# Optimization experiments

Measured on AMD Instinct MI355X. Metric: run time of the kernel, lower is better.

Reference implementation:

```python
import jax, jax.numpy as jnp
import numpy as np

H = 16  # num_heads

def _toroidal_bias(S, dtype):
    # float mask: +1.0 at (i, (i-1)%S), (i,i), (i, (i+1)%S); PyTorch ADDS float attn_mask to scores
    eye = jnp.eye(S, dtype=dtype)
    return eye + jnp.roll(eye, 1, axis=1) + jnp.roll(eye, -1, axis=1)

def setup_inputs() -> dict:
    key = jax.random.key(0)
    ks = jax.random.split(key, 7)
    E = 1024
    S, B = 2048, 2
    sc = 0.02
    return {
        "x": jax.random.normal(ks[0], (S, B, E), dtype=jnp.float32),
        "w_tor": jax.random.normal(ks[1], (E, E), dtype=jnp.float32) * sc,
        "b_tor": jax.random.normal(ks[2], (E,), dtype=jnp.float32) * sc,
        "in_proj_w": jax.random.normal(ks[3], (3 * E, E), dtype=jnp.float32) * sc,
        "in_proj_b": jax.random.normal(ks[4], (3 * E,), dtype=jnp.float32) * sc,
        "out_w": jax.random.normal(ks[5], (E, E), dtype=jnp.float32) * sc,
        "out_b": jax.random.normal(ks[6], (E,), dtype=jnp.float32) * sc,
    }

def reference(x, w_tor, b_tor, in_proj_w, in_proj_b, out_w, out_b):
    S, B, E = x.shape
    hd = E // H
    scale = 1.0 / jnp.sqrt(jnp.asarray(hd, dtype=x.dtype))
    # toroidal projection, then fused in_proj (self-attention: q=k=v=x_toroidal)
    xt = x @ w_tor.T + b_tor                      # (S,B,E)
    qkv = xt @ in_proj_w.T + in_proj_b            # (S,B,3E)
    q, k, v = jnp.split(qkv, 3, axis=-1)
    def to_heads(t):
        return t.reshape(S, B, H, hd).transpose(1, 2, 0, 3)  # (B,H,S,hd)
    q, k, v = to_heads(q), to_heads(k), to_heads(v)
    bias = _toroidal_bias(S, x.dtype)             # (S,S) additive float mask
    scores = jnp.einsum('bhqd,bhkd->bhqk', q * scale, k) + bias
    attn = jax.nn.softmax(scores, axis=-1)
    o = jnp.einsum('bhqk,bhkd->bhqd', attn, v)    # (B,H,S,hd)
    o = o.transpose(2, 0, 1, 3).reshape(S, B, E)
    return o @ out_w.T + out_b
```

## Files before the change

kernel.cpp:

```cpp
#include <hip/hip_runtime.h>

#define S_LEN 2048
#define NB    2
#define EMB   1024
#define NH    16
#define HD    64

typedef __bf16 bf16_t;
typedef bf16_t bf16x8 __attribute__((ext_vector_type(8)));
typedef bf16_t bf16x4v __attribute__((ext_vector_type(4)));
typedef float  f32x4  __attribute__((ext_vector_type(4)));
typedef float  f32x16 __attribute__((ext_vector_type(16)));

#define L2E 1.44269504f

__device__ __forceinline__ void g2l16(const void* g, void* l) {
    auto gp = reinterpret_cast<const unsigned int __attribute__((address_space(1)))*>(
        reinterpret_cast<uintptr_t>(g));
    auto lp = reinterpret_cast<unsigned int __attribute__((address_space(3)))*>(
        reinterpret_cast<uintptr_t>(l));
    __builtin_amdgcn_global_load_lds(gp, lp, 16, 0, 0);
}

__device__ __forceinline__ unsigned int pk2(float a, float b) {
    union { unsigned int u; bf16_t h[2]; } r;
    r.h[0] = (bf16_t)a; r.h[1] = (bf16_t)b;
    return r.u;
}

__global__ __launch_bounds__(256) void cast4_f32_bf16(
    const float* __restrict__ s0, bf16_t* __restrict__ d0,
    const float* __restrict__ s1, bf16_t* __restrict__ d1,
    const float* __restrict__ s2, bf16_t* __restrict__ d2,
    const float* __restrict__ s3, bf16_t* __restrict__ d3)
{
    long i = (long)blockIdx.x * 256 + threadIdx.x;
    const float* s; bf16_t* d; long off;
    if (i < 1048576)      { s = s0; d = d0; off = i; }
    else if (i < 1310720) { s = s1; d = d1; off = i - 1048576; }
    else if (i < 2097152) { s = s2; d = d2; off = i - 1310720; }
    else                  { s = s3; d = d3; off = i - 2097152; }
    float4 v = ((const float4*)s)[off];
    bf16x4v o;
    o[0] = (bf16_t)v.x; o[1] = (bf16_t)v.y; o[2] = (bf16_t)v.z; o[3] = (bf16_t)v.w;
    *(bf16x4v*)(d + off * 4) = o;
}

template<int TN, int MODE>
__global__ __launch_bounds__(256) void gemm_bt_bf16(
    const bf16_t* __restrict__ A, const bf16_t* __restrict__ W,
    const float* __restrict__ bias, void* __restrict__ Cout,
    bf16_t* __restrict__ Qp, bf16_t* __restrict__ Kp, bf16_t* __restrict__ Vtp,
    int M, int N, int K)
{
    constexpr int MB = (TN == 128) ? 4 : 2;
    __shared__ __align__(16) bf16_t As[2][128 * 32];
    __shared__ __align__(16) bf16_t Bs[2][TN * 32];

    const int tid  = threadIdx.x;
    const int lane = tid & 63;
    const int w    = tid >> 6;
    const int lm   = lane & 15;
    const int lq   = lane >> 4;
    const long m0  = (long)blockIdx.y * 128;
    const long n0  = (long)blockIdx.x * TN;
    const int wm0  = (TN == 128) ? (w >> 1) * 64 : w * 32;
    const int wn0  = (TN == 128) ? (w & 1) * 64 : 0;

    f32x4 acc[MB][4];
#pragma unroll
    for (int i = 0; i < MB; ++i)
#pragma unroll
        for (int j = 0; j < 4; ++j) acc[i][j] = (f32x4){0.f, 0.f, 0.f, 0.f};

    auto stage = [&](int k0, int buf) {
        bf16_t* asb = &As[buf][0];
        bf16_t* bsb = &Bs[buf][0];
#pragma unroll
        for (int j = 0; j < 2; ++j) {
            int a   = (w * 2 + j) * 64 + lane;
            int row = a >> 2;
            int c   = (a & 3) ^ ((row >> 1) & 3);
            g2l16(A + (m0 + row) * K + k0 + c * 8, asb + (w * 2 + j) * 512);
        }
#pragma unroll
        for (int j = 0; j < TN / 64; ++j) {
            int a   = (w * (TN / 64) + j) * 64 + lane;
            int row = a >> 2;
            int c   = (a & 3) ^ ((row >> 1) & 3);
            g2l16(W + (n0 + row) * K + k0 + c * 8, bsb + (w * (TN / 64) + j) * 512);
        }
    };

    stage(0, 0);
    for (int k0 = 0; k0 < K; k0 += 32) {
        const int cur = (k0 >> 5) & 1;
        asm volatile("s_waitcnt vmcnt(0)" ::: "memory");
        __syncthreads();
        if (k0 + 32 < K) stage(k0 + 32, cur ^ 1);

        bf16x8 af[MB], bfr[4];
#pragma unroll
        for (int mb = 0; mb < MB; ++mb) {
            int r = wm0 + mb * 16 + lm;
            af[mb] = *(const bf16x8*)&As[cur][r * 32 + ((lq ^ ((r >> 1) & 3)) << 3)];
        }
#pragma unroll
        for (int nb = 0; nb < 4; ++nb) {
            int r = wn0 + nb * 16 + lm;
            bfr[nb] = *(const bf16x8*)&Bs[cur][r * 32 + ((lq ^ ((r >> 1) & 3)) << 3)];
        }
#pragma unroll
        for (int mb = 0; mb < MB; ++mb)
#pragma unroll
            for (int nb = 0; nb < 4; ++nb)
                acc[mb][nb] = __builtin_amdgcn_mfma_f32_16x16x32_bf16(
                    af[mb], bfr[nb], acc[mb][nb], 0, 0, 0);
    }

    float b4[4];
#pragma unroll
    for (int nb = 0; nb < 4; ++nb) b4[nb] = bias[n0 + wn0 + nb * 16 + lm];

    if (MODE == 2) {
#pragma unroll
        for (int mb = 0; mb < MB; ++mb) {
            const long mbase = m0 + wm0 + mb * 16 + lq * 4;
#pragma unroll
            for (int nb = 0; nb < 4; ++nb) {
                int n    = (int)n0 + wn0 + nb * 16 + lm;
                int sec  = n >> 10;
                int nloc = n & 1023;
                int h    = nloc >> 6;
                int d    = nloc & 63;
                if (sec == 2) {
                    int s0 = (int)(mbase >> 1) + 0;
#pragma unroll
                    for (int rp = 0; rp < 2; ++rp) {
                        int bh = rp * 16 + h;
                        unsigned int pk = pk2(acc[mb][nb][rp] + b4[nb],
                                              acc[mb][nb][rp + 2] + b4[nb]);
                        *(unsigned int*)&Vtp[((size_t)(bh * 64 + d)) * S_LEN + s0] = pk;
                    }
                } else {
#pragma unroll
                    for (int r = 0; r < 4; ++r) {
                        long m  = mbase + r;
                        int  s  = (int)(m >> 1), b = (int)(m & 1);
                        int  bh = b * 16 + h;
                        float v = acc[mb][nb][r] + b4[nb];
                        if (sec == 0) {
                            Qp[((size_t)(bh * S_LEN + s)) * 64 + d] =
                                (bf16_t)(v * (0.125f * L2E));
                        } else {
                            Kp[((size_t)(bh * S_LEN + s)) * 64 + d] = (bf16_t)v;
                        }
                    }
                }
            }
        }
    } else {
#pragma unroll
        for (int mb = 0; mb < MB; ++mb) {
#pragma unroll
            for (int r = 0; r < 4; ++r) {
                long m = m0 + wm0 + mb * 16 + lq * 4 + r;
#pragma unroll
                for (int nb = 0; nb < 4; ++nb) {
                    int n   = (int)n0 + wn0 + nb * 16 + lm;
                    float v = acc[mb][nb][r] + b4[nb];
                    if (MODE == 0) ((float*)Cout)[m * N + n] = v;
                    else           ((bf16_t*)Cout)[m * N + n] = (bf16_t)v;
                }
            }
        }
    }
}

__global__ __launch_bounds__(256, 2) void attn_mfma(
    const bf16_t* __restrict__ Qb, const bf16_t* __restrict__ Kb,
    const bf16_t* __restrict__ Vtb, bf16_t* __restrict__ O)
{
    __shared__ __align__(16) bf16_t Ks[2][8 * 512];
    __shared__ __align__(16) bf16_t Vts[2][8 * 512];
    __shared__ __align__(16) bf16_t Ps[4][8 * 256];

    const int tid  = threadIdx.x;
    const int lane = tid & 63;
    const int w    = tid >> 6;
    const int bid  = blockIdx.x;
    const int bh   = ((bid & 7) << 2) | (bid >> 7);
    const int qt   = (bid >> 3) & 15;
    const int l5   = lane & 31;
    const int hi   = lane >> 5;

    const int rsub = lane >> 3;
    const int csw  = (lane & 7) ^ rsub;
    int cc[4];
#pragma unroll
    for (int i = 0; i < 4; ++i) cc[i] = ((2 * i + hi) ^ (l5 & 7)) * 8;

    const bf16_t* qrow = Qb + ((size_t)bh * S_LEN + qt * 128 + w * 32 + l5) * 64 + hi * 8;
    bf16x8 qf[4];
#pragma unroll
    for (int ds = 0; ds < 4; ++ds) qf[ds] = *(const bf16x8*)(qrow + ds * 16);

    f32x16 oacc[2];
#pragma unroll
    for (int dh = 0; dh < 2; ++dh)
#pragma unroll
        for (int i = 0; i < 16; ++i) oacc[dh][i] = 0.f;
    float plsum = 0.f;

    auto stageKV = [&](int kt, int buf) {
        bf16_t* ksb = &Ks[buf][0];
        bf16_t* vsb = &Vts[buf][0];
        const bf16_t* kg = Kb + ((size_t)bh * S_LEN + kt * 64) * 64;
        const bf16_t* vg = Vtb + (size_t)bh * 64 * S_LEN + kt * 64;
#pragma unroll
        for (int j = 0; j < 2; ++j) {
            int i = w * 2 + j;
            g2l16(kg + (size_t)(i * 8 + rsub) * 64 + csw * 8,    ksb + i * 512);
            g2l16(vg + (size_t)(i * 8 + rsub) * S_LEN + csw * 8, vsb + i * 512);
        }
    };

    stageKV(0, 0);
    for (int kt = 0; kt < 32; ++kt) {
        const int cur = kt & 1;
        asm volatile("s_waitcnt vmcnt(0)" ::: "memory");
        __syncthreads();
        if (kt < 31) stageKV(kt + 1, cur ^ 1);

        f32x16 sacc[2];
        __builtin_amdgcn_s_setprio(1);
#pragma unroll
        for (int kh = 0; kh < 2; ++kh) {
#pragma unroll
            for (int i = 0; i < 16; ++i) sacc[kh][i] = 0.f;
#pragma unroll
            for (int ds = 0; ds < 4; ++ds) {
                bf16x8 kf = *(const bf16x8*)&Ks[cur][(kh * 32 + l5) * 64 + cc[ds]];
                sacc[kh] = __builtin_amdgcn_mfma_f32_32x32x16_bf16(kf, qf[ds], sacc[kh], 0, 0, 0);
            }
        }
        __builtin_amdgcn_s_setprio(0);

        int ktd = (kt - 2 * qt) & 31;
        if (ktd <= 2 || ktd == 31) {
            int q = qt * 128 + w * 32 + l5;
#pragma unroll
            for (int kh = 0; kh < 2; ++kh)
#pragma unroll
                for (int r = 0; r < 16; ++r) {
                    int key  = kt * 64 + kh * 32 + (r & 3) + 8 * (r >> 2) + 4 * hi;
                    int diff = (key - q) & (S_LEN - 1);
                    if (diff <= 1 || diff == S_LEN - 1) sacc[kh][r] += L2E;
                }
        }

#pragma unroll
        for (int kh = 0; kh < 2; ++kh)
#pragma unroll
            for (int g = 0; g < 4; ++g) {
                bf16x4v pk;
#pragma unroll
                for (int e = 0; e < 4; ++e) {
                    float p = __builtin_amdgcn_exp2f(sacc[kh][g * 4 + e]);
                    plsum += p;
                    pk[e] = (bf16_t)p;
                }
                *(bf16x4v*)&Ps[w][(kh * 4 + g) * 256 + hi * 128 + l5 * 4] = pk;
            }

        bf16x8 pf[4];
#pragma unroll
        for (int ks = 0; ks < 4; ++ks) {
            bf16x4v lo = *(const bf16x4v*)&Ps[w][(2 * ks + hi) * 256 + l5 * 4];
            bf16x4v hb = *(const bf16x4v*)&Ps[w][(2 * ks + hi) * 256 + 128 + l5 * 4];
#pragma unroll
            for (int e = 0; e < 4; ++e) { pf[ks][e] = lo[e]; pf[ks][4 + e] = hb[e]; }
        }
        __builtin_amdgcn_s_setprio(1);
#pragma unroll
        for (int dh = 0; dh < 2; ++dh) {
#pragma unroll
            for (int ks = 0; ks < 4; ++ks) {
                bf16x8 vf = *(const bf16x8*)&Vts[cur][(dh * 32 + l5) * 64 + cc[ks]];
                oacc[dh] = __builtin_amdgcn_mfma_f32_32x32x16_bf16(pf[ks], vf, oacc[dh], 0, 0, 0);
            }
        }
        __builtin_amdgcn_s_setprio(0);
    }

    plsum += __shfl_xor(plsum, 32, 64);
    float* Lw = (float*)&Ps[w][0];
    if (hi == 0) Lw[l5] = plsum;

    float inv16[16];
#pragma unroll
    for (int g = 0; g < 4; ++g) {
        f32x4 lv = *(const f32x4*)&Lw[8 * g + 4 * hi];
#pragma unroll
        for (int e = 0; e < 4; ++e) inv16[g * 4 + e] = 1.0f / lv[e];
    }

    const int b = bh >> 4, h = bh & 15;
#pragma unroll
    for (int dh = 0; dh < 2; ++dh)
#pragma unroll
        for (int r = 0; r < 16; ++r) {
            int qrel = (r & 3) + 8 * (r >> 2) + 4 * hi;
            int s = qt * 128 + w * 32 + qrel;
            O[((size_t)(s * NB + b)) * EMB + h * 64 + dh * 32 + l5] =
                (bf16_t)(oacc[dh][r] * inv16[r]);
        }
}

extern "C" void kernel_launch(void* const* d_in, const int* in_sizes, int n_in,
                              void* d_out, int out_size, void* d_ws, size_t ws_size,
                              hipStream_t stream)
{
    const float* x         = (const float*)d_in[0];
    const float* w_tor     = (const float*)d_in[1];
    const float* b_tor     = (const float*)d_in[2];
    const float* in_proj_w = (const float*)d_in[3];
    const float* in_proj_b = (const float*)d_in[4];
    const float* out_w     = (const float*)d_in[5];
    const float* out_b     = (const float*)d_in[6];
    float* out = (float*)d_out;

    const int M = S_LEN * NB;

    char* base = (char*)d_ws;
    bf16_t* xb    = (bf16_t*)(base);
    bf16_t* wtorb = (bf16_t*)(base + ( 8ull << 20));
    bf16_t* ipwb  = (bf16_t*)(base + (10ull << 20));
    bf16_t* outwb = (bf16_t*)(base + (16ull << 20));
    bf16_t* xtb   = (bf16_t*)(base + (18ull << 20));
    bf16_t* Kb    = (bf16_t*)(base + (26ull << 20));
    bf16_t* Vtb   = (bf16_t*)(base + (34ull << 20));
    bf16_t* Qb    = xb;
    bf16_t* Ob    = xtb;

    cast4_f32_bf16<<<dim3(9216), 256, 0, stream>>>(
        x, xb, w_tor, wtorb, in_proj_w, ipwb, out_w, outwb);

    gemm_bt_bf16<64, 1><<<dim3(EMB / 64, M / 128), 256, 0, stream>>>(
        xb, wtorb, b_tor, xtb, nullptr, nullptr, nullptr, M, EMB, EMB);

    gemm_bt_bf16<128, 2><<<dim3(3 * EMB / 128, M / 128), 256, 0, stream>>>(
        xtb, ipwb, in_proj_b, nullptr, Qb, Kb, Vtb, M, 3 * EMB, EMB);

    attn_mfma<<<dim3(32 * 16), 256, 0, stream>>>(Qb, Kb, Vtb, Ob);

    gemm_bt_bf16<64, 0><<<dim3(EMB / 64, M / 128), 256, 0, stream>>>(
        Ob, outwb, out_b, out, nullptr, nullptr, nullptr, M, EMB, EMB);
}
```

Baseline: 208.9 us.

## Add dedicated 256x256-tile QKV projection GEMM with swizzled LDS and block remap

Replaces the generic 128x128-tile QKV projection with a specialised 512-thread kernel that computes 256x256 output tiles over a K-step of 64, using 128KB of dynamic shared memory, XOR-swizzled LDS layout, interleaved prefetch of the next tile and s_setprio around the MFMA bursts. Block indices are remapped so neighbouring blocks share A/W tiles in cache. The intent is higher arithmetic intensity and less global/LDS traffic for the largest GEMM. The cost is heavy register and LDS use and only 192 blocks, which may leave some CUs idle on a 256-CU part.

Measured after the change: 219.3 us. +5.0%, slower.

```diff
diff --git a/kernel.cpp b/kernel.cpp
--- a/kernel.cpp
+++ b/kernel.cpp
@@ -50,7 +50,6 @@
 __global__ __launch_bounds__(256) void gemm_bt_bf16(
     const bf16_t* __restrict__ A, const bf16_t* __restrict__ W,
     const float* __restrict__ bias, void* __restrict__ Cout,
-    bf16_t* __restrict__ Qp, bf16_t* __restrict__ Kp, bf16_t* __restrict__ Vtp,
     int M, int N, int K)
 {
     constexpr int MB = (TN == 128) ? 4 : 2;
@@ -122,55 +121,147 @@
 #pragma unroll
     for (int nb = 0; nb < 4; ++nb) b4[nb] = bias[n0 + wn0 + nb * 16 + lm];
 
-    if (MODE == 2) {
-#pragma unroll
-        for (int mb = 0; mb < MB; ++mb) {
-            const long mbase = m0 + wm0 + mb * 16 + lq * 4;
+#pragma unroll
+    for (int mb = 0; mb < MB; ++mb) {
+#pragma unroll
+        for (int r = 0; r < 4; ++r) {
+            long m = m0 + wm0 + mb * 16 + lq * 4 + r;
 #pragma unroll
             for (int nb = 0; nb < 4; ++nb) {
-                int n    = (int)n0 + wn0 + nb * 16 + lm;
-                int sec  = n >> 10;
-                int nloc = n & 1023;
-                int h    = nloc >> 6;
-                int d    = nloc & 63;
-                if (sec == 2) {
-                    int s0 = (int)(mbase >> 1) + 0;
-#pragma unroll
-                    for (int rp = 0; rp < 2; ++rp) {
-                        int bh = rp * 16 + h;
-                        unsigned int pk = pk2(acc[mb][nb][rp] + b4[nb],
-                                              acc[mb][nb][rp + 2] + b4[nb]);
-                        *(unsigned int*)&Vtp[((size_t)(bh * 64 + d)) * S_LEN + s0] = pk;
+                int n   = (int)n0 + wn0 + nb * 16 + lm;
+                float v = acc[mb][nb][r] + b4[nb];
+                if (MODE == 0) ((float*)Cout)[m * N + n] = v;
+                else           ((bf16_t*)Cout)[m * N + n] = (bf16_t)v;
+            }
+        }
+    }
+}
+
+__global__ __launch_bounds__(512, 2) void gemm_qkv_256(
+    const bf16_t* __restrict__ A, const bf16_t* __restrict__ W,
+    const float* __restrict__ bias,
+    bf16_t* __restrict__ Qp, bf16_t* __restrict__ Kp, bf16_t* __restrict__ Vtp)
+{
+    extern __shared__ __align__(16) char smem[];
+    bf16_t* AsB = (bf16_t*)smem;
+    bf16_t* BsB = (bf16_t*)(smem + 65536);
+
+    const int tid  = threadIdx.x;
+    const int lane = tid & 63;
+    const int w    = tid >> 6;
+    const int wr   = w >> 2;
+    const int wc   = w & 3;
+    const int lm   = lane & 15;
+    const int lq   = lane >> 4;
+    const int rs8  = lane >> 3;
+    const int csw  = (lane & 7) ^ rs8;
+
+    const int bid  = blockIdx.x;
+    const int swz  = (bid & 7) * 24 + (bid >> 3);
+    const long m0  = (long)(swz / 12) * 256;
+    const long n0  = (long)(swz % 12) * 256;
+
+    f32x4 acc[8][4];
+#pragma unroll
+    for (int i = 0; i < 8; ++i)
+#pragma unroll
+        for (int j = 0; j < 4; ++j) acc[i][j] = (f32x4){0.f, 0.f, 0.f, 0.f};
+
+    auto stageA = [&](int kt, int buf) {
+        bf16_t* dst = AsB + buf * 16384;
+        const bf16_t* src = A + (m0 + rs8) * 1024 + kt * 64 + csw * 8;
+#pragma unroll
+        for (int j = 0; j < 4; ++j) {
+            int iA = w * 4 + j;
+            g2l16(src + (size_t)iA * 8 * 1024, dst + iA * 512);
+        }
+    };
+    auto stageB = [&](int kt, int buf) {
+        bf16_t* dst = BsB + buf * 16384;
+        const bf16_t* src = W + (n0 + rs8) * 1024 + kt * 64 + csw * 8;
+#pragma unroll
+        for (int j = 0; j < 4; ++j) {
+            int iB = w * 4 + j;
+            g2l16(src + (size_t)iB * 8 * 1024, dst + iB * 512);
+        }
+    };
+
+    stageA(0, 0); stageB(0, 0);
+    stageA(1, 1); stageB(1, 1);
+    asm volatile("s_waitcnt vmcnt(8)" ::: "memory");
+    __syncthreads();
+
+    for (int t = 0; t < 16; ++t) {
+        const int cur = t & 1;
+        const bf16_t* Ac = AsB + cur * 16384;
+        const bf16_t* Bc = BsB + cur * 16384;
+        const bool st = (t >= 1) && (t < 15);
+
+#pragma unroll
+        for (int p = 0; p < 4; ++p) {
+            const int ks  = p >> 1;
+            const int mbh = p & 1;
+            bf16x8 af[4], bfq[4];
+#pragma unroll
+            for (int j = 0; j < 4; ++j) {
+                int rowA = wr * 128 + mbh * 64 + j * 16 + lm;
+                af[j]  = *(const bf16x8*)&Ac[rowA * 64 + (((ks * 4 + lq) ^ (lm & 7)) * 8)];
+                int rowB = wc * 64 + j * 16 + lm;
+                bfq[j] = *(const bf16x8*)&Bc[rowB * 64 + (((ks * 4 + lq) ^ (lm & 7)) * 8)];
+            }
+            if (p == 0 && st) stageA(t + 1, cur ^ 1);
+            if (p == 1 && st) stageB(t + 1, cur ^ 1);
+            __builtin_amdgcn_s_barrier();
+            __builtin_amdgcn_s_setprio(1);
+#pragma unroll
+            for (int j = 0; j < 4; ++j)
+#pragma unroll
+                for (int nb = 0; nb < 4; ++nb)
+                    acc[mbh * 4 + j][nb] = __builtin_amdgcn_mfma_f32_16x16x32_bf16(
+                        af[j], bfq[nb], acc[mbh * 4 + j][nb], 0, 0, 0);
+            __builtin_amdgcn_s_setprio(0);
+            __builtin_amdgcn_s_barrier();
+        }
+        asm volatile("s_waitcnt vmcnt(0)" ::: "memory");
+        __syncthreads();
+    }
+
+    float b4[4];
+#pragma unroll
+    for (int nb = 0; nb < 4; ++nb) b4[nb] = bias[n0 + wc * 64 + nb * 16 + lm];
+    const int sec = (int)(n0 >> 10);
+
+#pragma unroll
+    for (int mb = 0; mb < 8; ++mb) {
+        const long mbase = m0 + wr * 128 + mb * 16 + lq * 4;
+#pragma unroll
+        for (int nb = 0; nb < 4; ++nb) {
+            int n    = (int)n0 + wc * 64 + nb * 16 + lm;
+            int nloc = n & 1023;
+            int h    = nloc >> 6;
+            int d    = nloc & 63;
+            if (sec == 2) {
+                int s0 = (int)(mbase >> 1);
+#pragma unroll
+                for (int rp = 0; rp < 2; ++rp) {
+                    int bh = rp * 16 + h;
+                    unsigned int pkv = pk2(acc[mb][nb][rp]     + b4[nb],
+                                           acc[mb][nb][rp + 2] + b4[nb]);
+                    *(unsigned int*)&Vtp[((size_t)(bh * 64 + d)) * S_LEN + s0] = pkv;
+                }
+            } else {
+#pragma unroll
+                for (int r = 0; r < 4; ++r) {
+                    long m  = mbase + r;
+                    int  s  = (int)(m >> 1), b = (int)(m & 1);
+                    int  bh = b * 16 + h;
+                    float v = acc[mb][nb][r] + b4[nb];
+                    if (sec == 0) {
+                        Qp[((size_t)(bh * S_LEN + s)) * 64 + d] =
+                            (bf16_t)(v * (0.125f * L2E));
+                    } else {
+                        Kp[((size_t)(bh * S_LEN + s)) * 64 + d] = (bf16_t)v;
                     }
-                } else {
-#pragma unroll
-                    for (int r = 0; r < 4; ++r) {
-                        long m  = mbase + r;
-                        int  s  = (int)(m >> 1), b = (int)(m & 1);
-                        int  bh = b * 16 + h;
-                        float v = acc[mb][nb][r] + b4[nb];
-                        if (sec == 0) {
-                            Qp[((size_t)(bh * S_LEN + s)) * 64 + d] =
-                                (bf16_t)(v * (0.125f * L2E));
-                        } else {
-                            Kp[((size_t)(bh * S_LEN + s)) * 64 + d] = (bf16_t)v;
-                        }
-                    }
-                }
-            }
-        }
-    } else {
-#pragma unroll
-        for (int mb = 0; mb < MB; ++mb) {
-#pragma unroll
-            for (int r = 0; r < 4; ++r) {
-                long m = m0 + wm0 + mb * 16 + lq * 4 + r;
-#pragma unroll
-                for (int nb = 0; nb < 4; ++nb) {
-                    int n   = (int)n0 + wn0 + nb * 16 + lm;
-                    float v = acc[mb][nb][r] + b4[nb];
-                    if (MODE == 0) ((float*)Cout)[m * N + n] = v;
-                    else           ((bf16_t*)Cout)[m * N + n] = (bf16_t)v;
                 }
             }
         }
@@ -343,17 +434,20 @@
     bf16_t* Qb    = xb;
     bf16_t* Ob    = xtb;
 
+    hipFuncSetAttribute((const void*)gemm_qkv_256,
+                        hipFuncAttributeMaxDynamicSharedMemorySize, 131072);
+
     cast4_f32_bf16<<<dim3(9216), 256, 0, stream>>>(
         x, xb, w_tor, wtorb, in_proj_w, ipwb, out_w, outwb);
 
     gemm_bt_bf16<64, 1><<<dim3(EMB / 64, M / 128), 256, 0, stream>>>(
-        xb, wtorb, b_tor, xtb, nullptr, nullptr, nullptr, M, EMB, EMB);
-
-    gemm_bt_bf16<128, 2><<<dim3(3 * EMB / 128, M / 128), 256, 0, stream>>>(
-        xtb, ipwb, in_proj_b, nullptr, Qb, Kb, Vtb, M, 3 * EMB, EMB);
+        xb, wtorb, b_tor, xtb, M, EMB, EMB);
+
+    gemm_qkv_256<<<dim3(192), 512, 131072, stream>>>(
+        xtb, ipwb, in_proj_b, Qb, Kb, Vtb);
 
     attn_mfma<<<dim3(32 * 16), 256, 0, stream>>>(Qb, Kb, Vtb, Ob);
 
     gemm_bt_bf16<64, 0><<<dim3(EMB / 64, M / 128), 256, 0, stream>>>(
-        Ob, outwb, out_b, out, nullptr, nullptr, nullptr, M, EMB, EMB);
-}
+        Ob, outwb, out_b, out, M, EMB, EMB);
+}
```

## Permute V transpose layout so softmax P feeds PV MFMA from registers

Applied to the files above, without the earlier changes.

The QKV projection epilogue now writes V-transposed with a bit-permuted sequence index (swapping bits 2 and 3), so the key order matches the register layout of the score accumulators. The attention kernel then builds the PV MFMA operands directly from the exponentiated scores in registers, dropping the per-tile LDS round trip through the P buffer. This removes LDS writes and reads and shrinks shared memory, which may help occupancy. In exchange it couples the projection and attention kernels through a non-obvious key permutation that must stay consistent.

After: 208.1 us. About the same (-0.4%).

```diff
diff --git a/kernel.cpp b/kernel.cpp
--- a/kernel.cpp
+++ b/kernel.cpp
@@ -134,13 +134,14 @@
                 int h    = nloc >> 6;
                 int d    = nloc & 63;
                 if (sec == 2) {
-                    int s0 = (int)(mbase >> 1) + 0;
+                    int s0 = (int)(mbase >> 1);
+                    int sp = (s0 & ~12) | ((s0 & 4) << 1) | ((s0 & 8) >> 1);
 #pragma unroll
                     for (int rp = 0; rp < 2; ++rp) {
                         int bh = rp * 16 + h;
-                        unsigned int pk = pk2(acc[mb][nb][rp] + b4[nb],
-                                              acc[mb][nb][rp + 2] + b4[nb]);
-                        *(unsigned int*)&Vtp[((size_t)(bh * 64 + d)) * S_LEN + s0] = pk;
+                        unsigned int pkv = pk2(acc[mb][nb][rp]     + b4[nb],
+                                               acc[mb][nb][rp + 2] + b4[nb]);
+                        *(unsigned int*)&Vtp[((size_t)(bh * 64 + d)) * S_LEN + sp] = pkv;
                     }
                 } else {
 #pragma unroll
@@ -183,7 +184,7 @@
 {
     __shared__ __align__(16) bf16_t Ks[2][8 * 512];
     __shared__ __align__(16) bf16_t Vts[2][8 * 512];
-    __shared__ __align__(16) bf16_t Ps[4][8 * 256];
+    __shared__ __align__(16) float  Lw4[4][32];
 
     const int tid  = threadIdx.x;
     const int lane = tid & 63;
@@ -259,28 +260,24 @@
                 }
         }
 
+        float pv[2][16];
 #pragma unroll
         for (int kh = 0; kh < 2; ++kh)
 #pragma unroll
-            for (int g = 0; g < 4; ++g) {
-                bf16x4v pk;
-#pragma unroll
-                for (int e = 0; e < 4; ++e) {
-                    float p = __builtin_amdgcn_exp2f(sacc[kh][g * 4 + e]);
-                    plsum += p;
-                    pk[e] = (bf16_t)p;
-                }
-                *(bf16x4v*)&Ps[w][(kh * 4 + g) * 256 + hi * 128 + l5 * 4] = pk;
+            for (int i = 0; i < 16; ++i) {
+                pv[kh][i] = __builtin_amdgcn_exp2f(sacc[kh][i]);
+                plsum += pv[kh][i];
             }
 
         bf16x8 pf[4];
 #pragma unroll
         for (int ks = 0; ks < 4; ++ks) {
-            bf16x4v lo = *(const bf16x4v*)&Ps[w][(2 * ks + hi) * 256 + l5 * 4];
-            bf16x4v hb = *(const bf16x4v*)&Ps[w][(2 * ks + hi) * 256 + 128 + l5 * 4];
-#pragma unroll
-            for (int e = 0; e < 4; ++e) { pf[ks][e] = lo[e]; pf[ks][4 + e] = hb[e]; }
-        }
+            const int kh = ks >> 1, m = ks & 1;
+#pragma unroll
+            for (int e = 0; e < 8; ++e)
+                pf[ks][e] = (bf16_t)pv[kh][(e & 3) + 8 * m + 4 * (e >> 2)];
+        }
+
         __builtin_amdgcn_s_setprio(1);
 #pragma unroll
         for (int dh = 0; dh < 2; ++dh) {
@@ -294,13 +291,12 @@
     }
 
     plsum += __shfl_xor(plsum, 32, 64);
-    float* Lw = (float*)&Ps[w][0];
-    if (hi == 0) Lw[l5] = plsum;
+    if (hi == 0) Lw4[w][l5] = plsum;
 
     float inv16[16];
 #pragma unroll
     for (int g = 0; g < 4; ++g) {
-        f32x4 lv = *(const f32x4*)&Lw[8 * g + 4 * hi];
+        f32x4 lv = *(const f32x4*)&Lw4[w][8 * g + 4 * hi];
 #pragma unroll
         for (int e = 0; e < 4; ++e) inv16[g * 4 + e] = 1.0f / lv[e];
     }
```
